# Kernel tuning notes

Measured on AMD Instinct MI355X. Metric: run time of the kernel, lower is better.

## Reference

```python
import jax, jax.numpy as jnp
import numpy as np

C = 512        # num_channels
HEADS = 8      # num_channels // num_head_channels
DH = 64        # num_head_channels
G = 32         # num_groups
EPS = 1e-5
SCALE = DH ** -0.25  # pre-multiplied into q and k (scale applied twice -> 1/sqrt(DH))


def setup_inputs() -> dict:
    key = jax.random.key(0)
    ks = jax.random.split(key, 10)
    B, H, W = 2, 64, 64
    def w(k):
        return jax.random.normal(k, (C, C), jnp.float32) * 0.02
    def b(k):
        return jax.random.normal(k, (C,), jnp.float32) * 0.02
    return {
        "x": jax.random.normal(ks[0], (B, C, H, W), jnp.float32),
        "gn_w": jnp.ones((C,), jnp.float32),
        "gn_b": jnp.zeros((C,), jnp.float32),
        "wq": w(ks[1]), "bq": b(ks[2]),
        "wk": w(ks[3]), "bk": b(ks[4]),
        "wv": w(ks[5]), "bv": b(ks[6]),
        "wp": w(ks[7]), "bp": b(ks[8]),
    }


def reference(x, gn_w, gn_b, wq, bq, wk, bk, wv, bv, wp, bp):
    B, Cc, H, W = x.shape
    # GroupNorm over (C/G, H, W) per group
    xr = x.reshape(B, G, Cc // G, H * W)
    mean = xr.mean(axis=(2, 3), keepdims=True)
    var = xr.var(axis=(2, 3), keepdims=True)
    h = ((xr - mean) * jax.lax.rsqrt(var + EPS)).reshape(B, Cc, H, W)
    h = h * gn_w[None, :, None, None] + gn_b[None, :, None, None]
    # B C H W -> B (H W) C
    t = h.reshape(B, Cc, H * W).transpose(0, 2, 1)
    # q/k pre-multiplied by SCALE (equivalent to pre_multiply_weights_by_scale)
    q = (t @ wq.T + bq) * SCALE
    k = (t @ wk.T + bk) * SCALE
    v = t @ wv.T + bv
    def split_heads(a):  # B HW (h d) -> B h HW d
        return a.reshape(B, H * W, HEADS, DH).transpose(0, 2, 1, 3)
    q, k, v = split_heads(q), split_heads(k), split_heads(v)
    # full HWxHW score matrix, softmax over keys
    attn = jax.nn.softmax(jnp.einsum('bhqd,bhkd->bhqk', q, k), axis=-1)
    o = jnp.einsum('bhqk,bhkd->bhqd', attn, v)
    o = o.transpose(0, 2, 1, 3).reshape(B, H * W, Cc)  # join heads
    o = o @ wp.T + bp
    # B (H W) C -> B C H W, residual
    return o.transpose(0, 2, 1).reshape(B, Cc, H, W) + x
```

## Files before the change

### kernel.cpp

```cpp
#include <hip/hip_runtime.h>

#define HWN 4096
#define CCH 512
#define NHEAD 8
#define DHD 64
#define NBATCH 2
#define QK_SCALE 0.35355339059327373f
#define LOG2E    1.4426950408889634f

using floatx4 = __attribute__((ext_vector_type(4))) float;
using bf16x8  = __attribute__((ext_vector_type(8))) short;
using bf16x4  = __attribute__((ext_vector_type(4))) short;

__device__ __forceinline__ unsigned short f2b(float f) {
  union { float f; unsigned u; } x; x.f = f;
  unsigned r = x.u + 0x7FFFu + ((x.u >> 16) & 1u);
  return (unsigned short)(r >> 16);
}

__device__ __forceinline__ float b2f(unsigned short u) {
  union { unsigned u; float f; } x; x.u = ((unsigned)u) << 16;
  return x.f;
}

__device__ __forceinline__ float fast_exp2(float x) {
#if __has_builtin(__builtin_amdgcn_exp2f)
  return __builtin_amdgcn_exp2f(x);
#else
  return __expf(x * 0.69314718056f);
#endif
}

__device__ __forceinline__ unsigned pack_bf16_trunc(float lo, float hi) {
  return __builtin_amdgcn_perm(__float_as_uint(hi), __float_as_uint(lo), 0x07060302u);
}

__global__ __launch_bounds__(256) void gn_stats(const float* __restrict__ x,
                                                float* __restrict__ stat) {
  int bg = blockIdx.x;
  const float4* p = (const float4*)(x + (size_t)bg * 65536) + blockIdx.y * 2048;
  float s = 0.f, ss = 0.f;
  for (int i = threadIdx.x; i < 2048; i += 256) {
    float4 v = p[i];
    s  += v.x + v.y + v.z + v.w;
    ss += v.x*v.x + v.y*v.y + v.z*v.z + v.w*v.w;
  }
  for (int off = 32; off; off >>= 1) {
    s  += __shfl_xor(s, off);
    ss += __shfl_xor(ss, off);
  }
  __shared__ float red[8];
  int w = threadIdx.x >> 6;
  if ((threadIdx.x & 63) == 0) { red[w] = s; red[4 + w] = ss; }
  __syncthreads();
  if (threadIdx.x == 0) {
    float S  = red[0] + red[1] + red[2] + red[3];
    float SS = red[4] + red[5] + red[6] + red[7];
    atomicAdd(&stat[bg], S);
    atomicAdd(&stat[64 + bg], SS);
  }
}

__global__ __launch_bounds__(256) void prep_w(
    const float* __restrict__ wq, const float* __restrict__ wk,
    const float* __restrict__ wv, const float* __restrict__ wp,
    const float* __restrict__ bq, const float* __restrict__ bk,
    const float* __restrict__ bv,
    unsigned short* __restrict__ Wqkv, unsigned short* __restrict__ Wp,
    float* __restrict__ bqkv) {
  int i = blockIdx.x * 256 + threadIdx.x;
  if (i < 786432) {
    int row = i >> 9;
    float v;
    if (row < 512)       v = wq[i] * (QK_SCALE * LOG2E);
    else if (row < 1024) v = wk[i - 262144] * QK_SCALE;
    else                 v = wv[i - 524288];
    Wqkv[i] = f2b(v);
  } else if (i < 1048576) {
    Wp[i - 786432] = f2b(wp[i - 786432]);
  } else if (i < 1050112) {
    int j = i - 1048576;
    float v = (j < 512) ? bq[j] * (QK_SCALE * LOG2E)
            : (j < 1024) ? bk[j - 512] * QK_SCALE
            : bv[j - 1024];
    bqkv[j] = v;
  }
}

__global__ __launch_bounds__(256) void gn_apply(
    const float* __restrict__ x, const float* __restrict__ stat,
    const float* __restrict__ gnw, const float* __restrict__ gnb,
    unsigned short* __restrict__ t) {
  int pt = blockIdx.x & 63;
  int ct = (blockIdx.x >> 6) & 7;
  int b  = blockIdx.x >> 9;
  int c0 = ct * 64, p0 = pt * 64;
  __shared__ float tile[64][68];
  int tid = threadIdx.x;
  for (int pp = 0; pp < 4; ++pp) {
    int f = (pp * 256 + tid) * 4;
    int cl = f >> 6, pl = f & 63;
    int c = c0 + cl;
    float4 v = *(const float4*)(x + ((size_t)(b * 512 + c)) * 4096 + p0 + pl);
    int g = c >> 4;
    float S    = stat[b * 32 + g];
    float SS   = stat[64 + b * 32 + g];
    float mean = S * (1.f / 65536.f);
    float var  = SS * (1.f / 65536.f) - mean * mean;
    float rstd = rsqrtf(var + 1e-5f);
    float w  = gnw[c] * rstd;
    float bb = gnb[c] - mean * w;
    tile[cl][pl + 0] = v.x * w + bb;
    tile[cl][pl + 1] = v.y * w + bb;
    tile[cl][pl + 2] = v.z * w + bb;
    tile[cl][pl + 3] = v.w * w + bb;
  }
  __syncthreads();
  for (int pp = 0; pp < 2; ++pp) {
    int f = (pp * 256 + tid) * 8;
    int pl = f >> 6, cl = f & 63;
    unsigned short u[8];
#pragma unroll
    for (int j = 0; j < 8; ++j) u[j] = f2b(tile[cl + j][pl]);
    *(uint4*)(t + ((size_t)(b * 4096 + p0 + pl)) * 512 + c0 + cl) = *(uint4*)u;
  }
}

__global__ __launch_bounds__(256) void gemm_qkv(
    const unsigned short* __restrict__ t, const unsigned short* __restrict__ Wqkv,
    const float* __restrict__ bqkv,
    unsigned short* __restrict__ qo, unsigned short* __restrict__ Kp,
    unsigned short* __restrict__ vo) {
  int M0 = blockIdx.x * 64;
  int N0 = blockIdx.y * 64;
  __shared__ unsigned short At[64][72];
  __shared__ unsigned short Bt[64][72];
  int tid = threadIdx.x, w = tid >> 6, l = tid & 63;
  int quad = l >> 4, m16 = l & 15;
  floatx4 acc[4] = {};
  for (int k0 = 0; k0 < 512; k0 += 64) {
    __syncthreads();
#pragma unroll
    for (int pp = 0; pp < 2; ++pp) {
      int f = (pp * 256 + tid) * 8;
      int r = f >> 6, c = f & 63;
      *(uint4*)&At[r][c] = *(const uint4*)(t    + (size_t)(M0 + r) * 512 + k0 + c);
      *(uint4*)&Bt[r][c] = *(const uint4*)(Wqkv + (size_t)(N0 + r) * 512 + k0 + c);
    }
    __syncthreads();
    bf16x8 af0 = *(const bf16x8*)&At[w * 16 + m16][quad * 8];
    bf16x8 af1 = *(const bf16x8*)&At[w * 16 + m16][32 + quad * 8];
#pragma unroll
    for (int nt = 0; nt < 4; ++nt) {
      bf16x8 b0 = *(const bf16x8*)&Bt[nt * 16 + m16][quad * 8];
      bf16x8 b1 = *(const bf16x8*)&Bt[nt * 16 + m16][32 + quad * 8];
      acc[nt] = __builtin_amdgcn_mfma_f32_16x16x32_bf16(af0, b0, acc[nt], 0, 0, 0);
      acc[nt] = __builtin_amdgcn_mfma_f32_16x16x32_bf16(af1, b1, acc[nt], 0, 0, 0);
    }
  }
  int which = N0 >> 9;
  int head  = (N0 & 511) >> 6;
  if (which == 2) {
    __syncthreads();
#pragma unroll
    for (int nt = 0; nt < 4; ++nt) {
      int d = nt * 16 + m16;
      float bias = bqkv[N0 + d];
#pragma unroll
      for (int r = 0; r < 4; ++r)
        At[d][w * 16 + quad * 4 + r] = f2b(acc[nt][r] + bias);
    }
    __syncthreads();
    int bb = M0 >> 12, p0 = M0 & 4095;
    unsigned short* dst = vo + ((size_t)(bb * 8 + head) * 64) * 4096;
#pragma unroll
    for (int pp = 0; pp < 2; ++pp) {
      int f = (pp * 256 + tid) * 8;
      int d = f >> 6, pl = f & 63;
      *(uint4*)(dst + (size_t)d * 4096 + p0 + pl) = *(uint4*)&At[d][pl];
    }
  } else if (which == 1) {
    __syncthreads();
#pragma unroll
    for (int nt = 0; nt < 4; ++nt) {
      float bias = bqkv[N0 + nt * 16 + m16];
#pragma unroll
      for (int r = 0; r < 4; ++r)
        At[w * 16 + quad * 4 + r][nt * 16 + m16] = f2b(acc[nt][r] + bias);
    }
    __syncthreads();
    int bb = M0 >> 12, p = M0 & 4095;
    int kb = p >> 7, halfblk = (p >> 6) & 1;
    int ig = halfblk * 4 + w;
    int ntl = w >> 1, hh = w & 1;
    int row = ntl * 32 + hh * 4 + ((m16 >> 2) << 3) + (m16 & 3);
    size_t dstb = (((size_t)(bb * 8 + head) * 32 + kb) * 8 + ig) * 1024;
#pragma unroll
    for (int pp = 0; pp < 2; ++pp)
      *(uint4*)(Kp + dstb + pp * 512 + l * 8) = *(uint4*)&At[row][pp * 32 + quad * 8];
  } else {
#pragma unroll
    for (int nt = 0; nt < 4; ++nt) {
      int n = N0 + nt * 16 + m16;
      float bias = bqkv[n];
      int d = n & 63;
#pragma unroll
      for (int r = 0; r < 4; ++r) {
        int m = M0 + w * 16 + quad * 4 + r;
        int b = m >> 12, pp2 = m & 4095;
        qo[(((size_t)(b * 8 + head) * 4096 + pp2) << 6) + d] = f2b(acc[nt][r] + bias);
      }
    }
  }
}

__global__ __launch_bounds__(256, 4) void attn(
    const unsigned short* __restrict__ q, const unsigned short* __restrict__ Kp,
    const unsigned short* __restrict__ vt,
    unsigned short* __restrict__ pO, float* __restrict__ mlbuf) {
  int qt = blockIdx.x;
  int bh = blockIdx.y;
  int ks = blockIdx.z;
  __shared__ unsigned short Vt[64][136];
  int tid = threadIdx.x, w = tid >> 6, l = tid & 63;
  int quad = l >> 4, m16 = l & 15;
  const size_t vbase = (size_t)bh * HWN * DHD;
  const int key0 = ks * 2048;

  bf16x8 qf0, qf1;
  {
    int qrow = qt * 64 + w * 16 + m16;
    const unsigned short* qp = q + vbase + (size_t)qrow * 64 + quad * 8;
    qf0 = *(const bf16x8*)qp;
    qf1 = *(const bf16x8*)(qp + 32);
  }
  bf16x8 ones;
#pragma unroll
  for (int z = 0; z < 8; ++z) ones[z] = (short)0x3F80;

  floatx4 accO[4] = {};
  floatx4 accL = {};
  float mrow = -1e30f;

  for (int kt = 0; kt < 16; ++kt) {
    int kb = ks * 16 + kt;
    __syncthreads();
#pragma unroll
    for (int pp = 0; pp < 4; ++pp) {
      int f = (pp * 256 + tid) * 8;
      int rv = f >> 7, cv = f & 127;
      *(uint4*)&Vt[rv][cv] = *(const uint4*)(vt + vbase + (size_t)rv * 4096 + key0 + kt * 128 + cv);
    }
    __syncthreads();
    const unsigned short* kpb = Kp + (((size_t)bh * 32 + kb) * 8) * 1024 + l * 8;
    floatx4 s[8];
#pragma unroll
    for (int ig = 0; ig < 8; ++ig) {
      bf16x8 kf0 = *(const bf16x8*)(kpb + ig * 1024);
      bf16x8 kf1 = *(const bf16x8*)(kpb + ig * 1024 + 512);
      floatx4 z = {};
      z = __builtin_amdgcn_mfma_f32_16x16x32_bf16(kf0, qf0, z, 0, 0, 0);
      s[ig] = __builtin_amdgcn_mfma_f32_16x16x32_bf16(kf1, qf1, z, 0, 0, 0);
    }
    float mx = s[0][0];
#pragma unroll
    for (int ig = 0; ig < 8; ++ig)
#pragma unroll
      for (int i = 0; i < 4; ++i) mx = fmaxf(mx, s[ig][i]);
    mx = fmaxf(mx, __shfl_xor(mx, 16));
    mx = fmaxf(mx, __shfl_xor(mx, 32));
    bool grew = mx > mrow;
    float mnew = fmaxf(mrow, mx);
#pragma unroll
    for (int ig = 0; ig < 8; ++ig)
#pragma unroll
      for (int i = 0; i < 4; ++i)
        s[ig][i] = fast_exp2(s[ig][i] - mnew);
    if (__ballot(grew)) {
      float alpha = fast_exp2(mrow - mnew);
      float al0 = __shfl(alpha, quad * 4 + 0);
      float al1 = __shfl(alpha, quad * 4 + 1);
      float al2 = __shfl(alpha, quad * 4 + 2);
      float al3 = __shfl(alpha, quad * 4 + 3);
#pragma unroll
      for (int dt = 0; dt < 4; ++dt) {
        accO[dt][0] *= al0; accO[dt][1] *= al1;
        accO[dt][2] *= al2; accO[dt][3] *= al3;
      }
      accL[0] *= al0; accL[1] *= al1; accL[2] *= al2; accL[3] *= al3;
    }
    mrow = mnew;
    bf16x8 pf[4];
#pragma unroll
    for (int nt = 0; nt < 4; ++nt) {
      union { unsigned u[4]; bf16x8 v; } pu;
      pu.u[0] = pack_bf16_trunc(s[nt * 2][0],     s[nt * 2][1]);
      pu.u[1] = pack_bf16_trunc(s[nt * 2][2],     s[nt * 2][3]);
      pu.u[2] = pack_bf16_trunc(s[nt * 2 + 1][0], s[nt * 2 + 1][1]);
      pu.u[3] = pack_bf16_trunc(s[nt * 2 + 1][2], s[nt * 2 + 1][3]);
      pf[nt] = pu.v;
    }
#pragma unroll
    for (int dt = 0; dt < 4; ++dt) {
#pragma unroll
      for (int nt = 0; nt < 4; ++nt) {
        bf16x8 vf = *(const bf16x8*)&Vt[dt * 16 + m16][nt * 32 + quad * 8];
        accO[dt] = __builtin_amdgcn_mfma_f32_16x16x32_bf16(pf[nt], vf, accO[dt], 0, 0, 0);
      }
    }
#pragma unroll
    for (int nt = 0; nt < 4; ++nt)
      accL = __builtin_amdgcn_mfma_f32_16x16x32_bf16(pf[nt], ones, accL, 0, 0, 0);
  }
  const size_t prow = (size_t)(ks * 16 + bh) * 4096;
  float li0 = 1.f / accL[0];
  float li1 = 1.f / accL[1];
  float li2 = 1.f / accL[2];
  float li3 = 1.f / accL[3];
#pragma unroll
  for (int dt = 0; dt < 4; ++dt) {
    int d = dt * 16 + m16;
    int qrow = qt * 64 + w * 16 + quad * 4;
    size_t rb = (prow + qrow) * 64 + d;
    pO[rb]       = f2b(accO[dt][0] * li0);
    pO[rb + 64]  = f2b(accO[dt][1] * li1);
    pO[rb + 128] = f2b(accO[dt][2] * li2);
    pO[rb + 192] = f2b(accO[dt][3] * li3);
  }
  if (m16 < 4) {
    float mv = __shfl(mrow, quad * 4 + m16);
    float lv = (m16 == 0) ? accL[0] : (m16 == 1) ? accL[1] : (m16 == 2) ? accL[2] : accL[3];
    int qrow = qt * 64 + w * 16 + quad * 4 + m16;
    float2 v; v.x = mv; v.y = lv;
    ((float2*)mlbuf)[prow + qrow] = v;
  }
}

__global__ __launch_bounds__(256) void attn_merge(
    const unsigned short* __restrict__ pO, const float* __restrict__ mlbuf,
    unsigned short* __restrict__ ob) {
  int r = blockIdx.x * 64 + (threadIdx.x >> 2);
  int dseg = (threadIdx.x & 3) * 16;
  int bh = r >> 12, qq = r & 4095;
  int b = bh >> 3, h = bh & 7;
  const float2* mlp = (const float2*)mlbuf;
  float2 ml0 = mlp[r];
  float2 ml1 = mlp[65536 + r];
  float ms = fmaxf(ml0.x, ml1.x);
  float s0 = fast_exp2(ml0.x - ms) * ml0.y;
  float s1 = fast_exp2(ml1.x - ms) * ml1.y;
  float inv = 1.f / (s0 + s1);
  float w0 = s0 * inv, w1 = s1 * inv;
  const unsigned short* p0 = pO + ((size_t)r * 64 + dseg);
  const unsigned short* p1 = p0 + (size_t)65536 * 64;
  uint4 u0a = *(const uint4*)p0, u0b = *(const uint4*)(p0 + 8);
  uint4 u1a = *(const uint4*)p1, u1b = *(const uint4*)(p1 + 8);
  const unsigned short* a0 = (const unsigned short*)&u0a;
  const unsigned short* a1 = (const unsigned short*)&u1a;
  const unsigned short* b0p = (const unsigned short*)&u0b;
  const unsigned short* b1p = (const unsigned short*)&u1b;
  unsigned short u[16];
#pragma unroll
  for (int z = 0; z < 8; ++z) {
    u[z]     = f2b(w0 * b2f(a0[z])  + w1 * b2f(a1[z]));
    u[8 + z] = f2b(w0 * b2f(b0p[z]) + w1 * b2f(b1p[z]));
  }
  unsigned short* op = ob + ((size_t)(b * 4096 + qq)) * 512 + h * 64 + dseg;
  *(uint4*)op       = *(uint4*)u;
  *(uint4*)(op + 8) = *(uint4*)(u + 8);
}

__global__ __launch_bounds__(256) void gemm_out(
    const unsigned short* __restrict__ o, const unsigned short* __restrict__ Wp,
    const float* __restrict__ bp, const float* __restrict__ x,
    float* __restrict__ out) {
  int C0 = blockIdx.x * 64, P0 = blockIdx.y * 64, b = blockIdx.z;
  __shared__ unsigned short At[64][72];
  __shared__ unsigned short Bt[64][72];
  int tid = threadIdx.x, w = tid >> 6, l = tid & 63;
  int quad = l >> 4, m16 = l & 15;
  floatx4 acc[4] = {};
  for (int k0 = 0; k0 < 512; k0 += 64) {
    __syncthreads();
#pragma unroll
    for (int pp = 0; pp < 2; ++pp) {
      int f = (pp * 256 + tid) * 8;
      int r = f >> 6, c = f & 63;
      *(uint4*)&At[r][c] = *(const uint4*)(Wp + (size_t)(C0 + r) * 512 + k0 + c);
      *(uint4*)&Bt[r][c] = *(const uint4*)(o + ((size_t)(b * 4096 + P0 + r)) * 512 + k0 + c);
    }
    __syncthreads();
    bf16x8 af0 = *(const bf16x8*)&At[w * 16 + m16][quad * 8];
    bf16x8 af1 = *(const bf16x8*)&At[w * 16 + m16][32 + quad * 8];
#pragma unroll
    for (int nt = 0; nt < 4; ++nt) {
      bf16x8 b0 = *(const bf16x8*)&Bt[nt * 16 + m16][quad * 8];
      bf16x8 b1 = *(const bf16x8*)&Bt[nt * 16 + m16][32 + quad * 8];
      acc[nt] = __builtin_amdgcn_mfma_f32_16x16x32_bf16(af0, b0, acc[nt], 0, 0, 0);
      acc[nt] = __builtin_amdgcn_mfma_f32_16x16x32_bf16(af1, b1, acc[nt], 0, 0, 0);
    }
  }
#pragma unroll
  for (int r = 0; r < 4; ++r) {
    int c = C0 + w * 16 + quad * 4 + r;
    float bias = bp[c];
#pragma unroll
    for (int nt = 0; nt < 4; ++nt) {
      int p = P0 + nt * 16 + m16;
      size_t idx = ((size_t)(b * 512 + c)) * 4096 + p;
      out[idx] = acc[nt][r] + bias + x[idx];
    }
  }
}

extern "C" void kernel_launch(void* const* d_in, const int* in_sizes, int n_in,
                              void* d_out, int out_size, void* d_ws, size_t ws_size,
                              hipStream_t stream) {
  const float* x   = (const float*)d_in[0];
  const float* gnw = (const float*)d_in[1];
  const float* gnb = (const float*)d_in[2];
  const float* wq  = (const float*)d_in[3];
  const float* bq  = (const float*)d_in[4];
  const float* wk  = (const float*)d_in[5];
  const float* bk  = (const float*)d_in[6];
  const float* wv  = (const float*)d_in[7];
  const float* bv  = (const float*)d_in[8];
  const float* wp  = (const float*)d_in[9];
  const float* bp  = (const float*)d_in[10];
  float* out = (float*)d_out;

  char* ws = (char*)d_ws;
  float* stat          = (float*)ws;          ws += 1024;
  float* bqkv          = (float*)ws;          ws += 8192;
  unsigned short* Wqkv = (unsigned short*)ws; ws += (size_t)1536 * 512 * 2;
  unsigned short* Wp   = (unsigned short*)ws; ws += (size_t)512 * 512 * 2;
  unsigned short* t    = (unsigned short*)ws; ws += (size_t)8192 * 512 * 2;
  unsigned short* qb   = (unsigned short*)ws; ws += (size_t)8192 * 512 * 2;
  unsigned short* Kp   = (unsigned short*)ws; ws += (size_t)8192 * 512 * 2;
  unsigned short* vb   = (unsigned short*)ws; ws += (size_t)8192 * 512 * 2;
  unsigned short* ob   = (unsigned short*)ws; ws += (size_t)8192 * 512 * 2;

  unsigned short* pO  = (unsigned short*)d_out;
  float* mlbuf        = (float*)t;

  hipMemsetAsync(stat, 0, 512, stream);
  dim3 g0(64, 8);
  gn_stats<<<g0, 256, 0, stream>>>(x, stat);
  prep_w<<<4103, 256, 0, stream>>>(wq, wk, wv, wp, bq, bk, bv, Wqkv, Wp, bqkv);
  gn_apply<<<1024, 256, 0, stream>>>(x, stat, gnw, gnb, t);
  dim3 g1(128, 24);
  gemm_qkv<<<g1, 256, 0, stream>>>(t, Wqkv, bqkv, qb, Kp, vb);
  dim3 g2(64, 16, 2);
  attn<<<g2, 256, 0, stream>>>(qb, Kp, vb, pO, mlbuf);
  attn_merge<<<1024, 256, 0, stream>>>(pO, mlbuf, ob);
  dim3 g3(8, 64, 2);
  gemm_out<<<g3, 256, 0, stream>>>(ob, Wp, bp, x, out);
}
```

Before: 249.2 us.

## Double-buffer V tile via async global-to-LDS loads with XOR swizzle

The attention kernel now keeps two LDS buffers for the transposed V tile. While the current tile is used, the next one is prefetched with direct global_load_lds, which removes the register round-trip and one barrier per iteration. The padded layout is replaced by an XOR swizzle to avoid bank conflicts, and s_setprio raises priority around the MFMA sections. The cost is double the LDS for V, which may lower occupancy, plus correctness risk around async-load completion.

```diff
diff --git a/kernel.cpp b/kernel.cpp
--- a/kernel.cpp
+++ b/kernel.cpp
@@ -221,11 +221,21 @@
   int qt = blockIdx.x;
   int bh = blockIdx.y;
   int ks = blockIdx.z;
-  __shared__ unsigned short Vt[64][136];
+  __shared__ unsigned short Vt[2][64][128];
   int tid = threadIdx.x, w = tid >> 6, l = tid & 63;
   int quad = l >> 4, m16 = l & 15;
   const size_t vbase = (size_t)bh * HWN * DHD;
   const int key0 = ks * 2048;
+
+  int goff[4];
+#pragma unroll
+  for (int i = 0; i < 4; ++i) {
+    int c = w * 4 + i;
+    int row = 4 * c + (l >> 4);
+    int cbl = l & 15;
+    goff[i] = row * 4096 + ((cbl ^ (row & 15)) << 3);
+  }
+  const unsigned short* vtile = vt + vbase + key0;
 
   bf16x8 qf0, qf1;
   {
@@ -242,18 +252,32 @@
   floatx4 accL = {};
   float mrow = -1e30f;
 
+#pragma unroll
+  for (int i = 0; i < 4; ++i) {
+    __builtin_amdgcn_global_load_lds(
+        (const __attribute__((address_space(1))) unsigned int*)(vtile + goff[i]),
+        (__attribute__((address_space(3))) unsigned int*)(&Vt[0][0][0] + (w * 4 + i) * 512),
+        16, 0, 0);
+  }
+  __syncthreads();
+
   for (int kt = 0; kt < 16; ++kt) {
+    int cur = kt & 1;
     int kb = ks * 16 + kt;
-    __syncthreads();
-#pragma unroll
-    for (int pp = 0; pp < 4; ++pp) {
-      int f = (pp * 256 + tid) * 8;
-      int rv = f >> 7, cv = f & 127;
-      *(uint4*)&Vt[rv][cv] = *(const uint4*)(vt + vbase + (size_t)rv * 4096 + key0 + kt * 128 + cv);
-    }
-    __syncthreads();
+    if (kt < 15) {
+      const unsigned short* gp = vtile + (kt + 1) * 128;
+      unsigned short* lp = &Vt[cur ^ 1][0][0] + w * 4 * 512;
+#pragma unroll
+      for (int i = 0; i < 4; ++i) {
+        __builtin_amdgcn_global_load_lds(
+            (const __attribute__((address_space(1))) unsigned int*)(gp + goff[i]),
+            (__attribute__((address_space(3))) unsigned int*)(lp + i * 512),
+            16, 0, 0);
+      }
+    }
     const unsigned short* kpb = Kp + (((size_t)bh * 32 + kb) * 8) * 1024 + l * 8;
     floatx4 s[8];
+    __builtin_amdgcn_s_setprio(1);
 #pragma unroll
     for (int ig = 0; ig < 8; ++ig) {
       bf16x8 kf0 = *(const bf16x8*)(kpb + ig * 1024);
@@ -262,6 +286,7 @@
       z = __builtin_amdgcn_mfma_f32_16x16x32_bf16(kf0, qf0, z, 0, 0, 0);
       s[ig] = __builtin_amdgcn_mfma_f32_16x16x32_bf16(kf1, qf1, z, 0, 0, 0);
     }
+    __builtin_amdgcn_s_setprio(0);
     float mx = s[0][0];
 #pragma unroll
     for (int ig = 0; ig < 8; ++ig)
@@ -300,17 +325,20 @@
       pu.u[3] = pack_bf16_trunc(s[nt * 2 + 1][2], s[nt * 2 + 1][3]);
       pf[nt] = pu.v;
     }
+    __builtin_amdgcn_s_setprio(1);
 #pragma unroll
     for (int dt = 0; dt < 4; ++dt) {
 #pragma unroll
       for (int nt = 0; nt < 4; ++nt) {
-        bf16x8 vf = *(const bf16x8*)&Vt[dt * 16 + m16][nt * 32 + quad * 8];
+        bf16x8 vf = *(const bf16x8*)&Vt[cur][dt * 16 + m16][((nt * 4 + quad) ^ m16) << 3];
         accO[dt] = __builtin_amdgcn_mfma_f32_16x16x32_bf16(pf[nt], vf, accO[dt], 0, 0, 0);
       }
     }
 #pragma unroll
     for (int nt = 0; nt < 4; ++nt)
       accL = __builtin_amdgcn_mfma_f32_16x16x32_bf16(pf[nt], ones, accL, 0, 0, 0);
+    __builtin_amdgcn_s_setprio(0);
+    __syncthreads();
   }
   const size_t prow = (size_t)(ks * 16 + bh) * 4096;
   float li0 = 1.f / accL[0];
```

After: 268.2 us. 7.6% more time.

## Drop split-K attention and merge kernel; XOR-swizzle V tile in LDS

Applied to the files above, without the earlier changes.

The attention kernel now walks all 4096 keys in one block instead of splitting keys over two blocks, and writes normalized output straight into the head-joined layout. This removes the attn_merge kernel along with the partial-output and max/sum buffers. The V tile in shared memory loses its padding and uses an XOR swizzle to avoid bank conflicts. The grid shrinks from 2048 to 1024 blocks, which lowers parallelism and makes each block's serial key loop twice as long.

```diff
diff --git a/kernel.cpp b/kernel.cpp
--- a/kernel.cpp
+++ b/kernel.cpp
@@ -217,15 +217,13 @@
 __global__ __launch_bounds__(256, 4) void attn(
     const unsigned short* __restrict__ q, const unsigned short* __restrict__ Kp,
     const unsigned short* __restrict__ vt,
-    unsigned short* __restrict__ pO, float* __restrict__ mlbuf) {
+    unsigned short* __restrict__ ob) {
   int qt = blockIdx.x;
   int bh = blockIdx.y;
-  int ks = blockIdx.z;
-  __shared__ unsigned short Vt[64][136];
+  __shared__ unsigned short Vt[64][128];
   int tid = threadIdx.x, w = tid >> 6, l = tid & 63;
   int quad = l >> 4, m16 = l & 15;
   const size_t vbase = (size_t)bh * HWN * DHD;
-  const int key0 = ks * 2048;
 
   bf16x8 qf0, qf1;
   {
@@ -242,17 +240,17 @@
   floatx4 accL = {};
   float mrow = -1e30f;
 
-  for (int kt = 0; kt < 16; ++kt) {
-    int kb = ks * 16 + kt;
+  for (int kt = 0; kt < 32; ++kt) {
     __syncthreads();
 #pragma unroll
     for (int pp = 0; pp < 4; ++pp) {
       int f = (pp * 256 + tid) * 8;
       int rv = f >> 7, cv = f & 127;
-      *(uint4*)&Vt[rv][cv] = *(const uint4*)(vt + vbase + (size_t)rv * 4096 + key0 + kt * 128 + cv);
-    }
-    __syncthreads();
-    const unsigned short* kpb = Kp + (((size_t)bh * 32 + kb) * 8) * 1024 + l * 8;
+      uint4 v = *(const uint4*)(vt + vbase + (size_t)rv * 4096 + kt * 128 + cv);
+      *(uint4*)&Vt[rv][((cv >> 3) ^ (rv & 15)) << 3] = v;
+    }
+    __syncthreads();
+    const unsigned short* kpb = Kp + (((size_t)bh * 32 + kt) * 8) * 1024 + l * 8;
     floatx4 s[8];
 #pragma unroll
     for (int ig = 0; ig < 8; ++ig) {
@@ -304,7 +302,7 @@
     for (int dt = 0; dt < 4; ++dt) {
 #pragma unroll
       for (int nt = 0; nt < 4; ++nt) {
-        bf16x8 vf = *(const bf16x8*)&Vt[dt * 16 + m16][nt * 32 + quad * 8];
+        bf16x8 vf = *(const bf16x8*)&Vt[dt * 16 + m16][((nt * 4 + quad) ^ m16) << 3];
         accO[dt] = __builtin_amdgcn_mfma_f32_16x16x32_bf16(pf[nt], vf, accO[dt], 0, 0, 0);
       }
     }
@@ -312,62 +310,21 @@
     for (int nt = 0; nt < 4; ++nt)
       accL = __builtin_amdgcn_mfma_f32_16x16x32_bf16(pf[nt], ones, accL, 0, 0, 0);
   }
-  const size_t prow = (size_t)(ks * 16 + bh) * 4096;
+  int b = bh >> 3, h = bh & 7;
   float li0 = 1.f / accL[0];
   float li1 = 1.f / accL[1];
   float li2 = 1.f / accL[2];
   float li3 = 1.f / accL[3];
+  int qrow = qt * 64 + w * 16 + quad * 4;
+  unsigned short* op = ob + ((size_t)(b * 4096 + qrow)) * 512 + h * 64;
 #pragma unroll
   for (int dt = 0; dt < 4; ++dt) {
     int d = dt * 16 + m16;
-    int qrow = qt * 64 + w * 16 + quad * 4;
-    size_t rb = (prow + qrow) * 64 + d;
-    pO[rb]       = f2b(accO[dt][0] * li0);
-    pO[rb + 64]  = f2b(accO[dt][1] * li1);
-    pO[rb + 128] = f2b(accO[dt][2] * li2);
-    pO[rb + 192] = f2b(accO[dt][3] * li3);
-  }
-  if (m16 < 4) {
-    float mv = __shfl(mrow, quad * 4 + m16);
-    float lv = (m16 == 0) ? accL[0] : (m16 == 1) ? accL[1] : (m16 == 2) ? accL[2] : accL[3];
-    int qrow = qt * 64 + w * 16 + quad * 4 + m16;
-    float2 v; v.x = mv; v.y = lv;
-    ((float2*)mlbuf)[prow + qrow] = v;
-  }
-}
-
-__global__ __launch_bounds__(256) void attn_merge(
-    const unsigned short* __restrict__ pO, const float* __restrict__ mlbuf,
-    unsigned short* __restrict__ ob) {
-  int r = blockIdx.x * 64 + (threadIdx.x >> 2);
-  int dseg = (threadIdx.x & 3) * 16;
-  int bh = r >> 12, qq = r & 4095;
-  int b = bh >> 3, h = bh & 7;
-  const float2* mlp = (const float2*)mlbuf;
-  float2 ml0 = mlp[r];
-  float2 ml1 = mlp[65536 + r];
-  float ms = fmaxf(ml0.x, ml1.x);
-  float s0 = fast_exp2(ml0.x - ms) * ml0.y;
-  float s1 = fast_exp2(ml1.x - ms) * ml1.y;
-  float inv = 1.f / (s0 + s1);
-  float w0 = s0 * inv, w1 = s1 * inv;
-  const unsigned short* p0 = pO + ((size_t)r * 64 + dseg);
-  const unsigned short* p1 = p0 + (size_t)65536 * 64;
-  uint4 u0a = *(const uint4*)p0, u0b = *(const uint4*)(p0 + 8);
-  uint4 u1a = *(const uint4*)p1, u1b = *(const uint4*)(p1 + 8);
-  const unsigned short* a0 = (const unsigned short*)&u0a;
-  const unsigned short* a1 = (const unsigned short*)&u1a;
-  const unsigned short* b0p = (const unsigned short*)&u0b;
-  const unsigned short* b1p = (const unsigned short*)&u1b;
-  unsigned short u[16];
-#pragma unroll
-  for (int z = 0; z < 8; ++z) {
-    u[z]     = f2b(w0 * b2f(a0[z])  + w1 * b2f(a1[z]));
-    u[8 + z] = f2b(w0 * b2f(b0p[z]) + w1 * b2f(b1p[z]));
-  }
-  unsigned short* op = ob + ((size_t)(b * 4096 + qq)) * 512 + h * 64 + dseg;
-  *(uint4*)op       = *(uint4*)u;
-  *(uint4*)(op + 8) = *(uint4*)(u + 8);
+    op[d]         = f2b(accO[dt][0] * li0);
+    op[512 + d]   = f2b(accO[dt][1] * li1);
+    op[1024 + d]  = f2b(accO[dt][2] * li2);
+    op[1536 + d]  = f2b(accO[dt][3] * li3);
+  }
 }
 
 __global__ __launch_bounds__(256) void gemm_out(
@@ -440,9 +397,6 @@
   unsigned short* vb   = (unsigned short*)ws; ws += (size_t)8192 * 512 * 2;
   unsigned short* ob   = (unsigned short*)ws; ws += (size_t)8192 * 512 * 2;
 
-  unsigned short* pO  = (unsigned short*)d_out;
-  float* mlbuf        = (float*)t;
-
   hipMemsetAsync(stat, 0, 512, stream);
   dim3 g0(64, 8);
   gn_stats<<<g0, 256, 0, stream>>>(x, stat);
@@ -450,9 +404,8 @@
   gn_apply<<<1024, 256, 0, stream>>>(x, stat, gnw, gnb, t);
   dim3 g1(128, 24);
   gemm_qkv<<<g1, 256, 0, stream>>>(t, Wqkv, bqkv, qb, Kp, vb);
-  dim3 g2(64, 16, 2);
-  attn<<<g2, 256, 0, stream>>>(qb, Kp, vb, pO, mlbuf);
-  attn_merge<<<1024, 256, 0, stream>>>(pO, mlbuf, ob);
+  dim3 g2(64, 16);
+  attn<<<g2, 256, 0, stream>>>(qb, Kp, vb, ob);
   dim3 g3(8, 64, 2);
   gemm_out<<<g3, 256, 0, stream>>>(ob, Wp, bp, x, out);
 }
```

New measurement: 245.0 us. No clear change (-1.7%).
